# Kernel tuning notes

Measured on AMD Instinct MI355X. Metric: run time of the kernel, lower is better.

## Reference

```python
import jax, jax.numpy as jnp
import numpy as np

BN_EPS = 1e-5
K2 = 9  # 3x3 kernel


def _conv3x3(x, w, b):
    # x: [B,C,H,W], w: [O,C,3,3] -> [B,O,H,W], stride 1, pad 1
    out = jax.lax.conv_general_dilated(
        x, w, window_strides=(1, 1), padding=((1, 1), (1, 1)),
        dimension_numbers=("NCHW", "OIHW", "NCHW"))
    return out + b[None, :, None, None]


def setup_inputs() -> dict:
    key = jax.random.key(0)
    ks = jax.random.split(key, 8)
    B, C, H, W = 8, 256, 64, 64
    O = 256
    x = jax.random.normal(ks[0], (B, C, H, W), dtype=jnp.float32)
    # offset/mask conv: small init so sampled offsets stay near the base grid
    w_off = jax.random.normal(ks[1], (3 * K2, C, 3, 3), dtype=jnp.float32) * 0.01
    b_off = jnp.zeros((3 * K2,), dtype=jnp.float32)
    weight = jax.random.normal(ks[2], (O, C, 3, 3), dtype=jnp.float32) * 0.02
    bias = jnp.zeros((O,), dtype=jnp.float32)
    gamma = jnp.ones((O,), dtype=jnp.float32)
    beta = jnp.zeros((O,), dtype=jnp.float32)
    run_mean = jax.random.normal(ks[3], (O,), dtype=jnp.float32) * 0.1
    run_var = jax.random.uniform(ks[4], (O,), dtype=jnp.float32) + 0.5
    return {"x": x, "w_off": w_off, "b_off": b_off, "weight": weight,
            "bias": bias, "gamma": gamma, "beta": beta,
            "run_mean": run_mean, "run_var": run_var}


def _deform_sample(img, py, px):
    # img: [C,H,W]; py, px: [K2,H,W] sampling coordinates.
    # Bilinear sample with zero padding outside (DCNv2 semantics:
    # out-of-bounds corners contribute zero).
    C, H, W = img.shape
    y0 = jnp.floor(py)
    x0 = jnp.floor(px)
    wy1 = py - y0  # frac weights for the 'high' corner
    wx1 = px - x0

    def gather(yi, xi):
        valid = (yi >= 0) & (yi < H) & (xi >= 0) & (xi < W)
        yc = jnp.clip(yi, 0, H - 1).astype(jnp.int32)
        xc = jnp.clip(xi, 0, W - 1).astype(jnp.int32)
        return img[:, yc, xc] * valid.astype(img.dtype)[None]  # [C,K2,H,W]

    v00 = gather(y0, x0)
    v01 = gather(y0, x0 + 1)
    v10 = gather(y0 + 1, x0)
    v11 = gather(y0 + 1, x0 + 1)
    return (v00 * ((1 - wy1) * (1 - wx1))[None]
            + v01 * ((1 - wy1) * wx1)[None]
            + v10 * (wy1 * (1 - wx1))[None]
            + v11 * (wy1 * wx1)[None])  # [C,K2,H,W]


def reference(x, w_off, b_off, weight, bias, gamma, beta, run_mean, run_var):
    B, C, H, W = x.shape
    O = weight.shape[0]
    # 1) offset / mask branch (standard 3x3 conv)
    om = _conv3x3(x, w_off, b_off)  # [B, 27, H, W]
    off_y = om[:, :K2]
    off_x = om[:, K2:2 * K2]
    mask = jax.nn.sigmoid(om[:, 2 * K2:])  # modulation, [B,9,H,W]
    # 2) base sampling grid for 3x3, stride 1, pad 1, dilation 1
    ky = jnp.repeat(jnp.arange(3), 3).astype(x.dtype)  # [9]
    kx = jnp.tile(jnp.arange(3), 3).astype(x.dtype)    # [9]
    hs = jnp.arange(H, dtype=x.dtype)
    ws = jnp.arange(W, dtype=x.dtype)
    base_y = hs[None, :, None] - 1.0 + ky[:, None, None]  # [9,H,1]
    base_x = ws[None, None, :] - 1.0 + kx[:, None, None]  # [9,1,W]
    py = base_y[None] + off_y  # [B,9,H,W]
    px = base_x[None] + off_x
    # 3) modulated deformable im2col (bilinear gather) per batch
    cols = jax.vmap(_deform_sample)(x, py, px)  # [B,C,9,H,W]
    cols = cols * mask[:, None]                 # apply modulation mask
    # 4) GEMM over (C, K2) + bias
    w3 = weight.reshape(O, C, K2)
    out = jnp.einsum("ock,bckhw->bohw", w3, cols) + bias[None, :, None, None]
    # 5) BatchNorm (eval mode, running stats) + ReLU
    inv = gamma / jnp.sqrt(run_var + BN_EPS)
    out = out * inv[None, :, None, None] + (beta - run_mean * inv)[None, :, None, None]
    return jax.nn.relu(out)
```

## Files before the change

kernel.cpp:

```cpp
#include <hip/hip_runtime.h>
#include <math.h>

#define H 64
#define W 64
#define C 256
#define O 256
#define CK 2304
#define NB 8
#define HWSZ 4096

typedef __attribute__((ext_vector_type(8))) short short8;
typedef __attribute__((ext_vector_type(4))) float floatx4;
typedef __attribute__((ext_vector_type(4))) unsigned uintx4;

#define FSWZ(n) ((((n) & 3) << 1) | (((n) >> 2) & 1))

__device__ __forceinline__ unsigned short f2bf(float f) {
  unsigned u = __builtin_bit_cast(unsigned, f);
  unsigned r = (u + 0x7fffu + ((u >> 16) & 1u)) >> 16;
  return (unsigned short)r;
}
__device__ __forceinline__ float lo2f(unsigned u) {
  return __builtin_bit_cast(float, u << 16);
}
__device__ __forceinline__ float hi2f(unsigned u) {
  return __builtin_bit_cast(float, u & 0xffff0000u);
}
__device__ __forceinline__ unsigned pk2bf(float v0, float v1) {
  unsigned a = __builtin_bit_cast(unsigned, v0);
  unsigned b = __builtin_bit_cast(unsigned, v1);
  return ((a + 0x8000u) >> 16) | ((b + 0x8000u) & 0xffff0000u);
}

__global__ __launch_bounds__(256) void prep_all(
    const float* __restrict__ x, const float* __restrict__ weight,
    const float* __restrict__ w_off, const float* __restrict__ bias,
    const float* __restrict__ gamma, const float* __restrict__ beta,
    const float* __restrict__ run_mean, const float* __restrict__ run_var,
    unsigned short* __restrict__ xt, unsigned short* __restrict__ wb,
    unsigned short* __restrict__ wob, float* __restrict__ invsh) {
  __shared__ unsigned tile[64 * 65];
  int bid = blockIdx.x;
  int tid = threadIdx.x;

  if (bid < 1024) {
    int b = bid & 7;
    int t = bid >> 3;
    int y = t >> 1;
    int cg = t & 1;
    const float* xb = x + ((size_t)b * C + cg * 128) * HWSZ + y * W;
#pragma unroll
    for (int it = 0; it < 4; ++it) {
      int e = tid + 256 * it;
      int xx4 = e & 15;
      int cp = e >> 4;
      floatx4 f0 = *reinterpret_cast<const floatx4*>(
          xb + (size_t)(2 * cp) * HWSZ + xx4 * 4);
      floatx4 f1 = *reinterpret_cast<const floatx4*>(
          xb + (size_t)(2 * cp + 1) * HWSZ + xx4 * 4);
#pragma unroll
      for (int k = 0; k < 4; ++k)
        tile[cp * 65 + xx4 * 4 + k] = pk2bf(f0[k], f1[k]);
    }
    __syncthreads();
    unsigned short* xo = xt + ((size_t)(b * 64 + y) << 14) + cg * 128;
#pragma unroll
    for (int it = 0; it < 4; ++it) {
      int e = tid + 256 * it;
      int cq = e & 15;
      int xx = e >> 4;
      unsigned u0 = tile[(cq * 4 + 0) * 65 + xx];
      unsigned u1 = tile[(cq * 4 + 1) * 65 + xx];
      unsigned u2 = tile[(cq * 4 + 2) * 65 + xx];
      unsigned u3 = tile[(cq * 4 + 3) * 65 + xx];
      uint4 v = {u0, u1, u2, u3};
      *reinterpret_cast<uint4*>(xo + (xx << 8) + (cq << 3)) = v;
    }
  } else if (bid < 1312) {
    int d0 = ((bid - 1024) * 256 + tid) * 8;
    int lane = (d0 >> 3) & 63;
    int mt = (d0 >> 9) & 15;
    int ks = d0 >> 13;
    int o = mt * 16 + (lane & 15);
    int kn0 = ks * 32 + (lane >> 4) * 8;
    int tap = kn0 >> 8;
    int c0 = kn0 & 255;
    const float* wsrc = weight + o * CK + c0 * 9 + tap;
    unsigned pk[4];
#pragma unroll
    for (int p = 0; p < 4; ++p)
      pk[p] = pk2bf(wsrc[(2 * p) * 9], wsrc[(2 * p + 1) * 9]);
    uint4 v = {pk[0], pk[1], pk[2], pk[3]};
    *reinterpret_cast<uint4*>(wb + d0) = v;
  } else if (bid < 1348) {
    int d0 = ((bid - 1312) * 256 + tid) * 8;
    int lane = (d0 >> 3) & 63;
    int mt = (d0 >> 9) & 1;
    int ks = d0 >> 10;
    int o = mt * 16 + (lane & 15);
    int kn0 = ks * 32 + (lane >> 4) * 8;
    int tap = kn0 >> 8;
    int c0 = kn0 & 255;
    uint4 v;
    if (o < 27) {
      const float* wsrc = w_off + o * CK + c0 * 9 + tap;
      unsigned pk[4];
#pragma unroll
      for (int p = 0; p < 4; ++p)
        pk[p] = pk2bf(wsrc[(2 * p) * 9], wsrc[(2 * p + 1) * 9]);
      v = (uint4){pk[0], pk[1], pk[2], pk[3]};
    } else {
      v = (uint4){0, 0, 0, 0};
    }
    *reinterpret_cast<uint4*>(wob + d0) = v;
  } else {
    int o = tid;
    float inv = gamma[o] * rsqrtf(run_var[o] + 1e-5f);
    invsh[o] = inv;
    invsh[O + o] = beta[o] + (bias[o] - run_mean[o]) * inv;
  }
}

__global__ __launch_bounds__(512, 4) void deform_mfma_kernel(
    const unsigned short* __restrict__ xt, const unsigned short* __restrict__ wob,
    const float* __restrict__ b_off, const unsigned short* __restrict__ wb,
    const float* __restrict__ invsh, float* __restrict__ out) {
  __shared__ short cols[64 * 256];
  __shared__ float sm_om[27 * 64];
  __shared__ int sbase[576];
  __shared__ float s00[576], s01[576], s10[576], s11[576];

  int tid = threadIdx.x;
  int lane = tid & 63;
  int wvid = tid >> 6;
  int q = lane >> 4;
  int lm = lane & 15;
  int b = blockIdx.x;
  int h = blockIdx.y;
  const unsigned short* xtb = xt + ((size_t)b << 20);

  if (wvid < 4) {
    int mt = wvid & 1;
    int nh = wvid >> 1;
    floatx4 a0[2];
    a0[0] = (floatx4){0.f, 0.f, 0.f, 0.f};
    a0[1] = (floatx4){0.f, 0.f, 0.f, 0.f};
    int pxu[2];
    pxu[0] = (nh * 2 + 0) * 16 + lm;
    pxu[1] = (nh * 2 + 1) * 16 + lm;
    for (int tap = 0; tap < 9; ++tap) {
      int yy = h - 1 + tap / 3;
      bool vy = (yy >= 0) && (yy < H);
      const unsigned short* bp[2];
      bool vv[2];
#pragma unroll
      for (int u = 0; u < 2; ++u) {
        int xx = pxu[u] - 1 + tap % 3;
        vv[u] = vy && (xx >= 0) && (xx < W);
        bp[u] = xtb + ((((yy & 63) << 6) + (xx & 63)) << 8) + q * 8;
      }
#pragma unroll
      for (int s = 0; s < 8; ++s) {
        int ks = tap * 8 + s;
        short8 afrag = *reinterpret_cast<const short8*>(
            wob + (((ks * 2 + mt) * 64 + lane) << 3));
#pragma unroll
        for (int u = 0; u < 2; ++u) {
          short8 bfrag;
          if (vv[u])
            bfrag = *reinterpret_cast<const short8*>(bp[u] + s * 32);
          else
            bfrag = (short8){0, 0, 0, 0, 0, 0, 0, 0};
          a0[u] = __builtin_amdgcn_mfma_f32_16x16x32_bf16(afrag, bfrag, a0[u], 0, 0, 0);
        }
      }
    }
#pragma unroll
    for (int u = 0; u < 2; ++u)
#pragma unroll
      for (int r = 0; r < 4; ++r) {
        int o = mt * 16 + q * 4 + r;
        if (o < 27) sm_om[o * 64 + pxu[u]] = a0[u][r] + b_off[o];
      }
  }
  __syncthreads();

  for (int e = tid; e < 576; e += 512) {
    int n = e & 63;
    int k = e >> 6;
    float oy = sm_om[k * 64 + n];
    float ox = sm_om[(9 + k) * 64 + n];
    float mv = sm_om[(18 + k) * 64 + n];
    float m = 1.0f / (1.0f + __expf(-mv));
    float py = (float)(h - 1 + k / 3) + oy;
    float px = (float)(n - 1 + k % 3) + ox;
    float yf = floorf(py), xf = floorf(px);
    int y0 = (int)yf, x0 = (int)xf;
    float fy = py - yf, fx = px - xf;
    float r0, r1; int yl;
    if (y0 >= 0 && y0 <= H - 2)      { yl = y0;    r0 = 1.f - fy; r1 = fy;       }
    else if (y0 == -1)               { yl = 0;     r0 = fy;       r1 = 0.f;      }
    else if (y0 == H - 1)            { yl = H - 2; r0 = 0.f;      r1 = 1.f - fy; }
    else                             { yl = 0;     r0 = 0.f;      r1 = 0.f;      }
    float c0, c1; int xl;
    if (x0 >= 0 && x0 <= W - 2)      { xl = x0;    c0 = 1.f - fx; c1 = fx;       }
    else if (x0 == -1)               { xl = 0;     c0 = fx;       c1 = 0.f;      }
    else if (x0 == W - 1)            { xl = W - 2; c0 = 0.f;      c1 = 1.f - fx; }
    else                             { xl = 0;     c0 = 0.f;      c1 = 0.f;      }
    r0 *= m; r1 *= m;
    sbase[e] = ((yl << 6) + xl) << 8;
    s00[e] = r0 * c0; s01[e] = r0 * c1;
    s10[e] = r1 * c0; s11[e] = r1 * c1;
  }
  __syncthreads();

  floatx4 acc[2][4];
#pragma unroll
  for (int a = 0; a < 2; ++a)
#pragma unroll
    for (int u = 0; u < 4; ++u) acc[a][u] = (floatx4){0.f, 0.f, 0.f, 0.f};

  int sn = tid >> 3;
  int scb = tid & 7;

  for (int tap = 0; tap < 9; ++tap) {
    if (tap) __syncthreads();
    {
      int ei = tap * 64 + sn;
      int base = sbase[ei];
      float w00 = s00[ei], w01 = s01[ei], w10 = s10[ei], w11 = s11[ei];
      const unsigned short* p = xtb + base;
#pragma unroll
      for (int i = 0; i < 4; ++i) {
        int cbw = (i << 3) | scb;
        int co = cbw << 3;
        uintx4 u00 = *reinterpret_cast<const uintx4*>(p + co);
        uintx4 u01 = *reinterpret_cast<const uintx4*>(p + 256 + co);
        uintx4 u10 = *reinterpret_cast<const uintx4*>(p + 16384 + co);
        uintx4 u11 = *reinterpret_cast<const uintx4*>(p + 16640 + co);
        uintx4 res;
#pragma unroll
        for (int jd = 0; jd < 4; ++jd) {
          float v0 = fmaf(w00, lo2f(u00[jd]),
                     fmaf(w01, lo2f(u01[jd]),
                     fmaf(w10, lo2f(u10[jd]), w11 * lo2f(u11[jd]))));
          float v1 = fmaf(w00, hi2f(u00[jd]),
                     fmaf(w01, hi2f(u01[jd]),
                     fmaf(w10, hi2f(u10[jd]), w11 * hi2f(u11[jd]))));
          res[jd] = pk2bf(v0, v1);
        }
        int pos = (cbw ^ FSWZ(sn)) & 31;
        *reinterpret_cast<uintx4*>(&cols[(sn << 8) + (pos << 3)]) = res;
      }
    }
    __syncthreads();

#pragma unroll
    for (int s = 0; s < 8; ++s) {
      int ks = tap * 8 + s;
      short8 afrag[2];
#pragma unroll
      for (int a = 0; a < 2; ++a)
        afrag[a] = *reinterpret_cast<const short8*>(
            wb + (((ks * 16 + wvid * 2 + a) * 64 + lane) << 3));
      short8 bfrag[4];
#pragma unroll
      for (int u = 0; u < 4; ++u) {
        int nn = u * 16 + lm;
        int pos = ((s * 4 + q) ^ FSWZ(nn)) & 31;
        bfrag[u] = *reinterpret_cast<const short8*>(&cols[(nn << 8) + (pos << 3)]);
      }
#pragma unroll
      for (int a = 0; a < 2; ++a)
#pragma unroll
        for (int u = 0; u < 4; ++u)
          acc[a][u] = __builtin_amdgcn_mfma_f32_16x16x32_bf16(
              afrag[a], bfrag[u], acc[a][u], 0, 0, 0);
    }
  }

#pragma unroll
  for (int a = 0; a < 2; ++a) {
#pragma unroll
    for (int u = 0; u < 4; ++u) {
      int nn = u * 16 + lm;
#pragma unroll
      for (int r = 0; r < 4; ++r) {
        int o = (wvid * 2 + a) * 16 + q * 4 + r;
        float v = fmaf(acc[a][u][r], invsh[o], invsh[O + o]);
        out[((size_t)(b * O + o)) * HWSZ + h * W + nn] = fmaxf(v, 0.0f);
      }
    }
  }
}

extern "C" void kernel_launch(void* const* d_in, const int* in_sizes, int n_in,
                              void* d_out, int out_size, void* d_ws, size_t ws_size,
                              hipStream_t stream) {
  const float* x        = (const float*)d_in[0];
  const float* w_off    = (const float*)d_in[1];
  const float* b_off    = (const float*)d_in[2];
  const float* weight   = (const float*)d_in[3];
  const float* bias     = (const float*)d_in[4];
  const float* gamma    = (const float*)d_in[5];
  const float* beta     = (const float*)d_in[6];
  const float* run_mean = (const float*)d_in[7];
  const float* run_var  = (const float*)d_in[8];
  float* out = (float*)d_out;

  char* ws = (char*)d_ws;
  unsigned short* xt = (unsigned short*)ws;
  unsigned short* wbf = (unsigned short*)(ws + 16777216);
  unsigned short* wob = (unsigned short*)(ws + 17956864);
  float* invsh = (float*)(ws + 18104320);

  prep_all<<<1349, 256, 0, stream>>>(x, weight, w_off, bias, gamma, beta,
                                     run_mean, run_var, xt, wbf, wob, invsh);
  {
    dim3 grid(NB, H);
    deform_mfma_kernel<<<grid, 512, 0, stream>>>(xt, wob, b_off, wbf, invsh, out);
  }
}
```

Measured before the change: 192.5 us.

## Prefetch next-tap bilinear corners across MFMA, split offset conv over all waves

The bilinear gather loop is software pipelined. Half of the next tap's corner loads are issued into registers before the MFMA stage of the current tap, so global latency overlaps with matrix math, and the barrier moves to the end of each iteration. The offset/mask conv now uses all 8 waves with one 16-pixel tile each, instead of 4 waves doing two tiles each. Float-to-bf16 packing uses the gfx950 hardware cvt_pk_bf16_f32 instruction when it is available. The prefetch costs extra VGPRs under launch_bounds(512,4), and the hardware conversion may round differently from the manual packing.

```diff
diff --git a/kernel.cpp b/kernel.cpp
--- a/kernel.cpp
+++ b/kernel.cpp
@@ -15,11 +15,6 @@
 
 #define FSWZ(n) ((((n) & 3) << 1) | (((n) >> 2) & 1))
 
-__device__ __forceinline__ unsigned short f2bf(float f) {
-  unsigned u = __builtin_bit_cast(unsigned, f);
-  unsigned r = (u + 0x7fffu + ((u >> 16) & 1u)) >> 16;
-  return (unsigned short)r;
-}
 __device__ __forceinline__ float lo2f(unsigned u) {
   return __builtin_bit_cast(float, u << 16);
 }
@@ -30,6 +25,15 @@
   unsigned a = __builtin_bit_cast(unsigned, v0);
   unsigned b = __builtin_bit_cast(unsigned, v1);
   return ((a + 0x8000u) >> 16) | ((b + 0x8000u) & 0xffff0000u);
+}
+__device__ __forceinline__ unsigned cvtpk(float v0, float v1) {
+#if defined(__gfx950__) && __has_builtin(__builtin_amdgcn_cvt_pk_bf16_f32)
+  typedef __attribute__((ext_vector_type(2))) __bf16 bf16x2;
+  bf16x2 t = __builtin_amdgcn_cvt_pk_bf16_f32(v0, v1);
+  return __builtin_bit_cast(unsigned, t);
+#else
+  return pk2bf(v0, v1);
+#endif
 }
 
 __global__ __launch_bounds__(256) void prep_all(
@@ -60,7 +64,7 @@
           xb + (size_t)(2 * cp + 1) * HWSZ + xx4 * 4);
 #pragma unroll
       for (int k = 0; k < 4; ++k)
-        tile[cp * 65 + xx4 * 4 + k] = pk2bf(f0[k], f1[k]);
+        tile[cp * 65 + xx4 * 4 + k] = cvtpk(f0[k], f1[k]);
     }
     __syncthreads();
     unsigned short* xo = xt + ((size_t)(b * 64 + y) << 14) + cg * 128;
@@ -89,7 +93,7 @@
     unsigned pk[4];
 #pragma unroll
     for (int p = 0; p < 4; ++p)
-      pk[p] = pk2bf(wsrc[(2 * p) * 9], wsrc[(2 * p + 1) * 9]);
+      pk[p] = cvtpk(wsrc[(2 * p) * 9], wsrc[(2 * p + 1) * 9]);
     uint4 v = {pk[0], pk[1], pk[2], pk[3]};
     *reinterpret_cast<uint4*>(wb + d0) = v;
   } else if (bid < 1348) {
@@ -107,7 +111,7 @@
       unsigned pk[4];
 #pragma unroll
       for (int p = 0; p < 4; ++p)
-        pk[p] = pk2bf(wsrc[(2 * p) * 9], wsrc[(2 * p + 1) * 9]);
+        pk[p] = cvtpk(wsrc[(2 * p) * 9], wsrc[(2 * p + 1) * 9]);
       v = (uint4){pk[0], pk[1], pk[2], pk[3]};
     } else {
       v = (uint4){0, 0, 0, 0};
@@ -139,49 +143,35 @@
   int h = blockIdx.y;
   const unsigned short* xtb = xt + ((size_t)b << 20);
 
-  if (wvid < 4) {
+  {
     int mt = wvid & 1;
-    int nh = wvid >> 1;
-    floatx4 a0[2];
-    a0[0] = (floatx4){0.f, 0.f, 0.f, 0.f};
-    a0[1] = (floatx4){0.f, 0.f, 0.f, 0.f};
-    int pxu[2];
-    pxu[0] = (nh * 2 + 0) * 16 + lm;
-    pxu[1] = (nh * 2 + 1) * 16 + lm;
+    int nt = wvid >> 1;
+    floatx4 a0 = (floatx4){0.f, 0.f, 0.f, 0.f};
+    int px = nt * 16 + lm;
     for (int tap = 0; tap < 9; ++tap) {
       int yy = h - 1 + tap / 3;
-      bool vy = (yy >= 0) && (yy < H);
-      const unsigned short* bp[2];
-      bool vv[2];
-#pragma unroll
-      for (int u = 0; u < 2; ++u) {
-        int xx = pxu[u] - 1 + tap % 3;
-        vv[u] = vy && (xx >= 0) && (xx < W);
-        bp[u] = xtb + ((((yy & 63) << 6) + (xx & 63)) << 8) + q * 8;
-      }
+      int xx = px - 1 + tap % 3;
+      bool v = (yy >= 0) && (yy < H) && (xx >= 0) && (xx < W);
+      const unsigned short* bp =
+          xtb + ((((yy & 63) << 6) + (xx & 63)) << 8) + q * 8;
 #pragma unroll
       for (int s = 0; s < 8; ++s) {
         int ks = tap * 8 + s;
+        short8 bfrag;
+        if (v)
+          bfrag = *reinterpret_cast<const short8*>(bp + s * 32);
+        else
+          bfrag = (short8){0, 0, 0, 0, 0, 0, 0, 0};
         short8 afrag = *reinterpret_cast<const short8*>(
             wob + (((ks * 2 + mt) * 64 + lane) << 3));
-#pragma unroll
-        for (int u = 0; u < 2; ++u) {
-          short8 bfrag;
-          if (vv[u])
-            bfrag = *reinterpret_cast<const short8*>(bp[u] + s * 32);
-          else
-            bfrag = (short8){0, 0, 0, 0, 0, 0, 0, 0};
-          a0[u] = __builtin_amdgcn_mfma_f32_16x16x32_bf16(afrag, bfrag, a0[u], 0, 0, 0);
-        }
-      }
-    }
-#pragma unroll
-    for (int u = 0; u < 2; ++u)
-#pragma unroll
-      for (int r = 0; r < 4; ++r) {
-        int o = mt * 16 + q * 4 + r;
-        if (o < 27) sm_om[o * 64 + pxu[u]] = a0[u][r] + b_off[o];
-      }
+        a0 = __builtin_amdgcn_mfma_f32_16x16x32_bf16(afrag, bfrag, a0, 0, 0, 0);
+      }
+    }
+#pragma unroll
+    for (int r = 0; r < 4; ++r) {
+      int o = mt * 16 + q * 4 + r;
+      if (o < 27) sm_om[o * 64 + px] = a0[r] + b_off[o];
+    }
   }
   __syncthreads();
 
@@ -223,37 +213,80 @@
   int sn = tid >> 3;
   int scb = tid & 7;
 
+  uintx4 pf00[2], pf01[2], pf10[2], pf11[2];
+  {
+    const unsigned short* p0 = xtb + sbase[sn];
+#pragma unroll
+    for (int i = 0; i < 2; ++i) {
+      int co = ((i << 3) | scb) << 3;
+      pf00[i] = *reinterpret_cast<const uintx4*>(p0 + co);
+      pf01[i] = *reinterpret_cast<const uintx4*>(p0 + 256 + co);
+      pf10[i] = *reinterpret_cast<const uintx4*>(p0 + 16384 + co);
+      pf11[i] = *reinterpret_cast<const uintx4*>(p0 + 16640 + co);
+    }
+  }
+
   for (int tap = 0; tap < 9; ++tap) {
-    if (tap) __syncthreads();
-    {
-      int ei = tap * 64 + sn;
-      int base = sbase[ei];
-      float w00 = s00[ei], w01 = s01[ei], w10 = s10[ei], w11 = s11[ei];
-      const unsigned short* p = xtb + base;
-#pragma unroll
-      for (int i = 0; i < 4; ++i) {
-        int cbw = (i << 3) | scb;
-        int co = cbw << 3;
-        uintx4 u00 = *reinterpret_cast<const uintx4*>(p + co);
-        uintx4 u01 = *reinterpret_cast<const uintx4*>(p + 256 + co);
-        uintx4 u10 = *reinterpret_cast<const uintx4*>(p + 16384 + co);
-        uintx4 u11 = *reinterpret_cast<const uintx4*>(p + 16640 + co);
-        uintx4 res;
-#pragma unroll
-        for (int jd = 0; jd < 4; ++jd) {
-          float v0 = fmaf(w00, lo2f(u00[jd]),
-                     fmaf(w01, lo2f(u01[jd]),
-                     fmaf(w10, lo2f(u10[jd]), w11 * lo2f(u11[jd]))));
-          float v1 = fmaf(w00, hi2f(u00[jd]),
-                     fmaf(w01, hi2f(u01[jd]),
-                     fmaf(w10, hi2f(u10[jd]), w11 * hi2f(u11[jd]))));
-          res[jd] = pk2bf(v0, v1);
-        }
-        int pos = (cbw ^ FSWZ(sn)) & 31;
-        *reinterpret_cast<uintx4*>(&cols[(sn << 8) + (pos << 3)]) = res;
-      }
+    int ei = tap * 64 + sn;
+    float w00 = s00[ei], w01 = s01[ei], w10 = s10[ei], w11 = s11[ei];
+    const unsigned short* p = xtb + sbase[ei];
+
+    uintx4 t00[2], t01[2], t10[2], t11[2];
+#pragma unroll
+    for (int i = 0; i < 2; ++i) {
+      int co = (((i + 2) << 3) | scb) << 3;
+      t00[i] = *reinterpret_cast<const uintx4*>(p + co);
+      t01[i] = *reinterpret_cast<const uintx4*>(p + 256 + co);
+      t10[i] = *reinterpret_cast<const uintx4*>(p + 16384 + co);
+      t11[i] = *reinterpret_cast<const uintx4*>(p + 16640 + co);
+    }
+#pragma unroll
+    for (int i = 0; i < 2; ++i) {
+      int cbw = (i << 3) | scb;
+      uintx4 res;
+#pragma unroll
+      for (int jd = 0; jd < 4; ++jd) {
+        float v0 = fmaf(w00, lo2f(pf00[i][jd]),
+                   fmaf(w01, lo2f(pf01[i][jd]),
+                   fmaf(w10, lo2f(pf10[i][jd]), w11 * lo2f(pf11[i][jd]))));
+        float v1 = fmaf(w00, hi2f(pf00[i][jd]),
+                   fmaf(w01, hi2f(pf01[i][jd]),
+                   fmaf(w10, hi2f(pf10[i][jd]), w11 * hi2f(pf11[i][jd]))));
+        res[jd] = cvtpk(v0, v1);
+      }
+      int pos = (cbw ^ FSWZ(sn)) & 31;
+      *reinterpret_cast<uintx4*>(&cols[(sn << 8) + (pos << 3)]) = res;
+    }
+#pragma unroll
+    for (int i = 0; i < 2; ++i) {
+      int cbw = ((i + 2) << 3) | scb;
+      uintx4 res;
+#pragma unroll
+      for (int jd = 0; jd < 4; ++jd) {
+        float v0 = fmaf(w00, lo2f(t00[i][jd]),
+                   fmaf(w01, lo2f(t01[i][jd]),
+                   fmaf(w10, lo2f(t10[i][jd]), w11 * lo2f(t11[i][jd]))));
+        float v1 = fmaf(w00, hi2f(t00[i][jd]),
+                   fmaf(w01, hi2f(t01[i][jd]),
+                   fmaf(w10, hi2f(t10[i][jd]), w11 * hi2f(t11[i][jd]))));
+        res[jd] = cvtpk(v0, v1);
+      }
+      int pos = (cbw ^ FSWZ(sn)) & 31;
+      *reinterpret_cast<uintx4*>(&cols[(sn << 8) + (pos << 3)]) = res;
     }
     __syncthreads();
+
+    if (tap < 8) {
+      const unsigned short* pn = xtb + sbase[ei + 64];
+#pragma unroll
+      for (int i = 0; i < 2; ++i) {
+        int co = ((i << 3) | scb) << 3;
+        pf00[i] = *reinterpret_cast<const uintx4*>(pn + co);
+        pf01[i] = *reinterpret_cast<const uintx4*>(pn + 256 + co);
+        pf10[i] = *reinterpret_cast<const uintx4*>(pn + 16384 + co);
+        pf11[i] = *reinterpret_cast<const uintx4*>(pn + 16640 + co);
+      }
+    }
 
 #pragma unroll
     for (int s = 0; s < 8; ++s) {
@@ -277,6 +310,7 @@
           acc[a][u] = __builtin_amdgcn_mfma_f32_16x16x32_bf16(
               afrag[a], bfrag[u], acc[a][u], 0, 0, 0);
     }
+    __syncthreads();
   }
 
 #pragma unroll
```

Measured after the change: 209.9 us. +9.0%, slower.
